# Performance work log

Measured on AMD Instinct MI355X. Metric: run time of the kernel, lower is better.

Reference implementation:

```python
import jax, jax.numpy as jnp
import numpy as np

KSIZE = 7
PAD = KSIZE // 2          # reflection pad radius
EPS_BN = 1e-5             # CONFIG.model.arch.batchnorm_eps
SCALE = 1.0               # self.scale
BN_W, BN_B = 0.1, 0.0     # BatchNorm init per module


def _l2n(x, eps=1e-12):
    return x / (jnp.linalg.norm(x) + eps)


def setup_inputs() -> dict:
    key = jax.random.key(0)
    ks = jax.random.split(key, 6)
    B, Cg, Co, H, W = 2, 128, 32, 512, 512
    f = jax.random.normal(ks[0], (B, Cg, H, W), jnp.float32)
    alpha = jax.random.normal(ks[1], (B, Co, H, W), jnp.float32)
    # guidance_conv: 1x1 conv Cg -> Cg//2 (xavier-ish init)
    wg = jax.random.normal(ks[2], (Cg // 2, Cg), jnp.float32) * (1.0 / np.sqrt(Cg))
    bg = jnp.zeros((Cg // 2,), jnp.float32)
    # spectral-norm 1x1 conv Co -> Co, no bias
    w_bar = jax.random.normal(ks[3], (Co, Co), jnp.float32) * (1.0 / np.sqrt(Co))
    u = _l2n(jax.random.normal(ks[4], (Co,), jnp.float32))
    v = _l2n(jax.random.normal(ks[5], (Co,), jnp.float32))
    return {"f": f, "alpha": alpha, "wg": wg, "bg": bg, "w_bar": w_bar, "u": u, "v": v}


def reference(f, alpha, wg, bg, w_bar, u, v):
    B, _, H, W = f.shape
    # 1x1 guidance conv
    g = jnp.einsum('oc,bchw->bohw', wg, f) + bg[None, :, None, None]
    # hop_normalize: channel-wise L2 normalize, clamped at 1e-4
    gn = g / jnp.maximum(jnp.linalg.norm(g, axis=1, keepdims=True), 1e-4)
    r = jnp.pad(gn, ((0, 0), (0, 0), (PAD, PAD), (PAD, PAD)), mode='reflect')
    # ksize^2 shifted-window correlation -> scores [K2, B, 1, H, W]
    scores = []
    for i in range(KSIZE):
        for j in range(KSIZE):
            if i == PAD and j == PAD:
                scores.append(jnp.full((B, 1, H, W), -10000.0, gn.dtype))
            else:
                scores.append((gn * r[:, :, i:i + H, j:j + W]).sum(axis=1, keepdims=True))
    s = jax.nn.softmax(jnp.stack(scores, axis=0) * SCALE, axis=0)
    # weighted neighborhood aggregation of alpha (skip center tap)
    alp = jnp.pad(alpha, ((0, 0), (0, 0), (PAD, PAD), (PAD, PAD)), mode='reflect')
    y = jnp.zeros_like(alpha)
    for i in range(KSIZE):
        for j in range(KSIZE):
            if i == PAD and j == PAD:
                continue
            y = y + alp[:, :, i:i + H, j:j + W] * s[i * KSIZE + j]
    # spectral-norm 1x1 conv (training: one detached power iteration)
    v1 = jax.lax.stop_gradient(_l2n(w_bar.T @ u))
    u1 = jax.lax.stop_gradient(_l2n(w_bar @ v1))
    sigma = u1 @ (w_bar @ v1)
    w_sn = w_bar / sigma
    y2 = jnp.einsum('oc,bchw->bohw', w_sn, y)
    # BatchNorm2d, training mode (batch stats), weight=0.1 bias=0
    mean = y2.mean(axis=(0, 2, 3), keepdims=True)
    var = y2.var(axis=(0, 2, 3), keepdims=True)
    y_bn = BN_W * (y2 - mean) / jnp.sqrt(var + EPS_BN) + BN_B
    return y_bn + alpha
```

## Files before the change

### kernel.cpp

```cpp
#include <hip/hip_runtime.h>

#define HWc   262144
#define CGc   128
#define CHc   64
#define COc   32
#define NPIXc 524288
#define TW 32
#define TH 8
#define HLW 38
#define HLH 14
#define HPX (HLW*HLH)

typedef _Float16 h2 __attribute__((ext_vector_type(2)));

__device__ __forceinline__ int refl(int p){
  if (p < 0) p = -p;
  else if (p >= 512) p = 1022 - p;
  return p;
}
__device__ __forceinline__ h2 as_h2(unsigned u){ union{unsigned u; h2 h;} x; x.u = u; return x.h; }
__device__ __forceinline__ unsigned as_u(h2 h){ union{unsigned u; h2 h;} x; x.h = h; return x.u; }
__device__ __forceinline__ unsigned pkh(float a, float b){
  h2 h; h.x = (_Float16)a; h.y = (_Float16)b; return as_u(h);
}
__device__ __forceinline__ float2 upk(unsigned u){
  h2 h = as_h2(u); return make_float2((float)h.x, (float)h.y);
}
__device__ __forceinline__ float dot2h(unsigned a, unsigned b, float c){
  return __builtin_amdgcn_fdot2(as_h2(a), as_h2(b), c, false);
}
__device__ __forceinline__ void mixlo(float& acc, unsigned ab, float e){
  asm("v_fma_mix_f32 %0, %1, %2, %0 op_sel:[0,0,0] op_sel_hi:[1,0,0]"
      : "+v"(acc) : "v"(ab), "v"(e));
}
__device__ __forceinline__ void mixhi(float& acc, unsigned ab, float e){
  asm("v_fma_mix_f32 %0, %1, %2, %0 op_sel:[1,0,0] op_sel_hi:[1,0,0]"
      : "+v"(acc) : "v"(ab), "v"(e));
}

__global__ void k0_prep(const float* __restrict__ wbar, const float* __restrict__ u,
                        const float* __restrict__ wg,
                        unsigned* __restrict__ wsnb, unsigned* __restrict__ wgb){
  const int t = threadIdx.x;
  __shared__ float sv1[32];
  float tv = 0.f;
  if (t < 32){
    #pragma unroll
    for (int o = 0; o < 32; o++) tv += wbar[o*32 + t] * u[o];
  }
  float sq = tv * tv;
  #pragma unroll
  for (int off = 32; off; off >>= 1) sq += __shfl_down(sq, off);
  const float n1 = sqrtf(__shfl(sq, 0)) + 1e-12f;
  if (t < 32) sv1[t] = tv / n1;
  __syncthreads();
  float tu = 0.f;
  if (t < 32){
    #pragma unroll
    for (int c = 0; c < 32; c++) tu += wbar[t*32 + c] * sv1[c];
  }
  float sq2 = tu * tu;
  #pragma unroll
  for (int off = 32; off; off >>= 1) sq2 += __shfl_down(sq2, off);
  const float S = __shfl(sq2, 0);
  const float inv = (sqrtf(S) + 1e-12f) / S;
  for (int k = t; k < 512; k += 64){
    const int o = k >> 4, p = k & 15;
    wsnb[k] = pkh(wbar[o*32 + 2*p] * inv, wbar[o*32 + 2*p + 1] * inv);
  }
  for (int k = t; k < 4096; k += 64){
    const int o = k >> 6, p = k & 63;
    wgb[k] = pkh(wg[o*128 + 2*p], wg[o*128 + 2*p + 1]);
  }
}

__global__ __launch_bounds__(256) void k1f(const float* __restrict__ f,
                                           const float* __restrict__ alpha,
                                           const unsigned* __restrict__ wgb,
                                           const unsigned* __restrict__ wsnb,
                                           const float* __restrict__ bg,
                                           unsigned* __restrict__ gn,
                                           unsigned* __restrict__ apm){
  const int p   = blockIdx.x * 256 + threadIdx.x;
  const int b   = p >> 18;
  const int pix = p & (HWc - 1);
  const float* fb = f + (size_t)b * CGc * HWc + pix;

  float acc[CHc];
  #pragma unroll
  for (int o = 0; o < CHc; o++) acc[o] = bg[o];

  #pragma unroll 1
  for (int pp = 0; pp < 64; pp += 4){
    unsigned fp[4];
    #pragma unroll
    for (int m = 0; m < 4; m++)
      fp[m] = pkh(fb[(size_t)(2*(pp+m)) * HWc], fb[(size_t)(2*(pp+m)+1) * HWc]);
    #pragma unroll
    for (int o = 0; o < CHc; o++){
      float a = acc[o];
      a = dot2h(fp[0], wgb[o*64 + pp + 0], a);
      a = dot2h(fp[1], wgb[o*64 + pp + 1], a);
      a = dot2h(fp[2], wgb[o*64 + pp + 2], a);
      a = dot2h(fp[3], wgb[o*64 + pp + 3], a);
      acc[o] = a;
    }
  }
  float nsq = 0.f;
  #pragma unroll
  for (int o = 0; o < CHc; o++) nsq = fmaf(acc[o], acc[o], nsq);
  const float inv = 1.f / fmaxf(sqrtf(nsq), 1e-4f);

  uint4* gp = (uint4*)(gn + (size_t)p * 32);
  #pragma unroll
  for (int k = 0; k < 8; k++){
    uint4 w;
    w.x = pkh(acc[8*k+0]*inv, acc[8*k+1]*inv);
    w.y = pkh(acc[8*k+2]*inv, acc[8*k+3]*inv);
    w.z = pkh(acc[8*k+4]*inv, acc[8*k+5]*inv);
    w.w = pkh(acc[8*k+6]*inv, acc[8*k+7]*inv);
    gp[k] = w;
  }

  const float* ab = alpha + (size_t)b * COc * HWc + pix;
  unsigned a16[16];
  #pragma unroll
  for (int k = 0; k < 16; k++)
    a16[k] = pkh(ab[(size_t)(2*k) * HWc], ab[(size_t)(2*k+1) * HWc]);
  unsigned ow[16];
  #pragma unroll
  for (int o = 0; o < COc; o += 2){
    float s0 = 0.f, s1 = 0.f;
    #pragma unroll
    for (int k = 0; k < 16; k++){
      s0 = dot2h(a16[k], wsnb[(o+0)*16 + k], s0);
      s1 = dot2h(a16[k], wsnb[(o+1)*16 + k], s1);
    }
    ow[o >> 1] = pkh(s0, s1);
  }
  uint4* op = (uint4*)(apm + (size_t)p * 16);
  #pragma unroll
  for (int k = 0; k < 4; k++)
    op[k] = make_uint4(ow[4*k], ow[4*k+1], ow[4*k+2], ow[4*k+3]);
}

__global__ __launch_bounds__(256) void k2_agg(const unsigned* __restrict__ gn,
                                              const unsigned* __restrict__ apm,
                                              unsigned* __restrict__ y2){
  __shared__ uint4 gs4[8][HPX];

  const int lb  = (blockIdx.x & 7) * 256 + (blockIdx.x >> 3);
  const int txx = lb & 15;
  const int tyy = (lb >> 4) & 63;
  const int bb  = lb >> 10;
  const int x0  = txx * TW, y0 = tyy * TH;
  const int tid = threadIdx.x;

  for (int t = tid; t < HPX; t += 256){
    const int hr = t / HLW;
    const int hc = t - hr * HLW;
    const int gy = refl(y0 + hr - 3);
    const int gx = refl(x0 + hc - 3);
    const uint4* src = (const uint4*)(gn + (size_t)((bb << 18) + (gy << 9) + gx) * 32);
    #pragma unroll
    for (int k = 0; k < 8; k++) gs4[k][t] = src[k];
  }
  __syncthreads();

  const int r  = tid >> 5, c = tid & 31;
  const int yy = y0 + r,  xx = x0 + c;
  const int self = (r + 3) * HLW + (c + 3);

  uint4 cv[8];
  #pragma unroll
  for (int k = 0; k < 8; k++) cv[k] = gs4[k][self];

  int ax[7];
  #pragma unroll
  for (int j = 0; j < 7; j++) ax[j] = refl(xx + j - 3);

  float yac[COc];
  #pragma unroll
  for (int k = 0; k < COc; k++) yac[k] = 0.f;
  float esum = 0.f;

  #pragma unroll 1
  for (int i = 0; i < 7; i++){
    const int ay = refl(yy + i - 3);
    const unsigned* aprow = apm + (size_t)((bb << 18) + (ay << 9)) * 16;
    const int rowbase = (r + i) * HLW + c;
    #pragma unroll
    for (int j = 0; j < 7; j++){
      if (i == 3 && j == 3) continue;
      const int hp = rowbase + j;
      float s0 = 0.f, s1 = 0.f, s2 = 0.f, s3 = 0.f;
      #pragma unroll
      for (int k = 0; k < 8; k++){
        const uint4 q = gs4[k][hp];
        s0 = dot2h(cv[k].x, q.x, s0);
        s1 = dot2h(cv[k].y, q.y, s1);
        s2 = dot2h(cv[k].z, q.z, s2);
        s3 = dot2h(cv[k].w, q.w, s3);
      }
      const float e = __expf((s0 + s1) + (s2 + s3));
      esum += e;
      const uint4* ap = (const uint4*)(aprow + (size_t)ax[j] * 16);
      #pragma unroll
      for (int kk = 0; kk < 4; kk++){
        const uint4 a = ap[kk];
        mixlo(yac[8*kk+0], a.x, e); mixhi(yac[8*kk+1], a.x, e);
        mixlo(yac[8*kk+2], a.y, e); mixhi(yac[8*kk+3], a.y, e);
        mixlo(yac[8*kk+4], a.z, e); mixhi(yac[8*kk+5], a.z, e);
        mixlo(yac[8*kk+6], a.w, e); mixhi(yac[8*kk+7], a.w, e);
      }
    }
  }

  const float inv = 1.f / esum;
  unsigned yw[16];
  #pragma unroll
  for (int k = 0; k < 16; k++) yw[k] = pkh(yac[2*k] * inv, yac[2*k+1] * inv);
  uint4* yp = (uint4*)(y2 + (size_t)((bb << 18) + (yy << 9) + xx) * 16);
  #pragma unroll
  for (int k = 0; k < 4; k++)
    yp[k] = make_uint4(yw[4*k], yw[4*k+1], yw[4*k+2], yw[4*k+3]);
}

__global__ __launch_bounds__(256) void k3_stats(const unsigned* __restrict__ y2,
                                                float* __restrict__ stats){
  float s[COc], q[COc];
  #pragma unroll
  for (int o = 0; o < COc; o++){ s[o] = 0.f; q[o] = 0.f; }
  const int stride = gridDim.x * 256;
  for (int p = blockIdx.x * 256 + threadIdx.x; p < NPIXc; p += stride){
    const uint4* yp = (const uint4*)(y2 + (size_t)p * 16);
    #pragma unroll
    for (int k = 0; k < 4; k++){
      const uint4 w = yp[k];
      const unsigned vv[4] = {w.x, w.y, w.z, w.w};
      #pragma unroll
      for (int m = 0; m < 4; m++){
        const float2 ab = upk(vv[m]);
        s[8*k+2*m]   += ab.x; q[8*k+2*m]   = fmaf(ab.x, ab.x, q[8*k+2*m]);
        s[8*k+2*m+1] += ab.y; q[8*k+2*m+1] = fmaf(ab.y, ab.y, q[8*k+2*m+1]);
      }
    }
  }
  #pragma unroll
  for (int o = 0; o < COc; o++){
    #pragma unroll
    for (int off = 32; off; off >>= 1){
      s[o] += __shfl_down(s[o], off);
      q[o] += __shfl_down(q[o], off);
    }
  }
  __shared__ float red[4][64];
  const int wv = threadIdx.x >> 6;
  if ((threadIdx.x & 63) == 0){
    #pragma unroll
    for (int o = 0; o < COc; o++){ red[wv][o] = s[o]; red[wv][32 + o] = q[o]; }
  }
  __syncthreads();
  if (threadIdx.x < 64){
    const float v = red[0][threadIdx.x] + red[1][threadIdx.x]
                  + red[2][threadIdx.x] + red[3][threadIdx.x];
    atomicAdd(&stats[threadIdx.x], v);
  }
}

__global__ void k3b_final(const float* __restrict__ stats, float* __restrict__ stats2){
  const int t = threadIdx.x;
  if (t < COc){
    const float invN = 1.f / (float)NPIXc;
    const float mean = stats[t] * invN;
    const float var  = fmaf(-mean, mean, stats[COc + t] * invN);
    stats2[t]       = mean;
    stats2[COc + t] = 0.1f * rsqrtf(var + 1e-5f);
  }
}

__global__ __launch_bounds__(256) void k4_out(const unsigned* __restrict__ y2,
                                              const float* __restrict__ alpha,
                                              const float* __restrict__ stats2,
                                              float* __restrict__ out){
  const int p   = blockIdx.x * 256 + threadIdx.x;
  const int b   = p >> 18;
  const int pix = p & (HWc - 1);
  const uint4* yp = (const uint4*)(y2 + (size_t)p * 16);
  const size_t boff = (size_t)b * COc * HWc + pix;
  #pragma unroll
  for (int k = 0; k < 4; k++){
    const uint4 w = yp[k];
    const unsigned vv[4] = {w.x, w.y, w.z, w.w};
    #pragma unroll
    for (int m = 0; m < 4; m++){
      const int o = 8*k + 2*m;
      const float2 ab = upk(vv[m]);
      out[boff + (size_t)o*HWc]     = fmaf(ab.x - stats2[o],   stats2[COc+o],
                                           alpha[boff + (size_t)o*HWc]);
      out[boff + (size_t)(o+1)*HWc] = fmaf(ab.y - stats2[o+1], stats2[COc+o+1],
                                           alpha[boff + (size_t)(o+1)*HWc]);
    }
  }
}

extern "C" void kernel_launch(void* const* d_in, const int* in_sizes, int n_in,
                              void* d_out, int out_size, void* d_ws, size_t ws_size,
                              hipStream_t stream){
  const float* f     = (const float*)d_in[0];
  const float* alpha = (const float*)d_in[1];
  const float* wg    = (const float*)d_in[2];
  const float* bg    = (const float*)d_in[3];
  const float* wbar  = (const float*)d_in[4];
  const float* u     = (const float*)d_in[5];
  (void)in_sizes; (void)n_in; (void)out_size; (void)ws_size;
  float* out = (float*)d_out;

  char* ws = (char*)d_ws;
  float*    stats  = (float*)ws;
  float*    stats2 = (float*)(ws + 4096);
  unsigned* wsnb   = (unsigned*)(ws + 8192);
  unsigned* wgb    = (unsigned*)(ws + 16384);
  unsigned* apm    = (unsigned*)(ws + 65536);
  unsigned* gn     = (unsigned*)(ws + 65536 + (size_t)NPIXc*64);
  unsigned* y2     = (unsigned*)(ws + 65536 + (size_t)NPIXc*64 + (size_t)NPIXc*128);

  hipMemsetAsync(stats, 0, 64 * sizeof(float), stream);
  k0_prep  <<<1, 64, 0, stream>>>(wbar, u, wg, wsnb, wgb);
  k1f      <<<NPIXc / 256, 256, 0, stream>>>(f, alpha, wgb, wsnb, bg, gn, apm);
  k2_agg   <<<2048, 256, 0, stream>>>(gn, apm, y2);
  k3_stats <<<256, 256, 0, stream>>>(y2, stats);
  k3b_final<<<1, 64, 0, stream>>>(stats, stats2);
  k4_out   <<<NPIXc / 256, 256, 0, stream>>>(y2, alpha, stats2, out);
}
```

Before: 328.3 us.

## Compute guidance and spectral-norm 1x1 convs with MFMA in k1

Replaces the per-thread fdot2 loops for the 128->64 guidance conv and the 32x32 spectral-norm conv with 16x16x32 f16 MFMA instructions. Weights are pre-swizzled into MFMA A-operand layout in k0_prep and held in registers, each wave processes 16-pixel tiles, and the channel L2 norm is reduced across lanes with shuffles. This removes the heavy VALU and scalar-weight-load cost of the per-pixel matvec, at the price of strided per-lane loads of f and alpha with only 16 contiguous pixels per row and narrower (uint2) output stores. It also switches the fp32-to-fp16 conversion of the inputs to round-toward-zero.

Measured after the change: 326.3 us. Within noise of the previous version (-0.6%).

```diff
diff --git a/kernel.cpp b/kernel.cpp
--- a/kernel.cpp
+++ b/kernel.cpp
@@ -11,7 +11,12 @@
 #define HLH 14
 #define HPX (HLW*HLH)
 
-typedef _Float16 h2 __attribute__((ext_vector_type(2)));
+typedef _Float16 h2    __attribute__((ext_vector_type(2)));
+typedef __fp16   fp2   __attribute__((ext_vector_type(2)));
+typedef _Float16 f16x8 __attribute__((ext_vector_type(8)));
+typedef float    f32x4 __attribute__((ext_vector_type(4)));
+
+union AB { uint4 q; f16x8 v; h2 p[4]; unsigned u[4]; };
 
 __device__ __forceinline__ int refl(int p){
   if (p < 0) p = -p;
@@ -23,6 +28,9 @@
 __device__ __forceinline__ unsigned pkh(float a, float b){
   h2 h; h.x = (_Float16)a; h.y = (_Float16)b; return as_u(h);
 }
+__device__ __forceinline__ h2 pkrtz(float a, float b){
+  union{ fp2 f; h2 h; } x; x.f = __builtin_amdgcn_cvt_pkrtz(a, b); return x.h;
+}
 __device__ __forceinline__ float2 upk(unsigned u){
   h2 h = as_h2(u); return make_float2((float)h.x, (float)h.y);
 }
@@ -40,7 +48,7 @@
 
 __global__ void k0_prep(const float* __restrict__ wbar, const float* __restrict__ u,
                         const float* __restrict__ wg,
-                        unsigned* __restrict__ wsnb, unsigned* __restrict__ wgb){
+                        unsigned* __restrict__ wgA, unsigned* __restrict__ wsnA){
   const int t = threadIdx.x;
   __shared__ float sv1[32];
   float tv = 0.f;
@@ -64,84 +72,107 @@
   for (int off = 32; off; off >>= 1) sq2 += __shfl_down(sq2, off);
   const float S = __shfl(sq2, 0);
   const float inv = (sqrtf(S) + 1e-12f) / S;
+
+  for (int k = t; k < 4096; k += 64){
+    const int mk = k >> 8, L = (k >> 2) & 63, j = k & 3;
+    const int m = mk >> 2, ks = mk & 3;
+    const int o = m*16 + (L & 15);
+    const int c = ks*32 + 8*(L >> 4) + 2*j;
+    wgA[k] = pkh(wg[o*128 + c], wg[o*128 + c + 1]);
+  }
   for (int k = t; k < 512; k += 64){
-    const int o = k >> 4, p = k & 15;
-    wsnb[k] = pkh(wbar[o*32 + 2*p] * inv, wbar[o*32 + 2*p + 1] * inv);
-  }
-  for (int k = t; k < 4096; k += 64){
-    const int o = k >> 6, p = k & 63;
-    wgb[k] = pkh(wg[o*128 + 2*p], wg[o*128 + 2*p + 1]);
-  }
-}
-
-__global__ __launch_bounds__(256) void k1f(const float* __restrict__ f,
+    const int m = k >> 8, L = (k >> 2) & 63, j = k & 3;
+    const int o = m*16 + (L & 15);
+    const int c = 8*(L >> 4) + 2*j;
+    wsnA[k] = pkh(wbar[o*32 + c] * inv, wbar[o*32 + c + 1] * inv);
+  }
+}
+
+__global__ __launch_bounds__(256) void k1m(const float* __restrict__ f,
                                            const float* __restrict__ alpha,
-                                           const unsigned* __restrict__ wgb,
-                                           const unsigned* __restrict__ wsnb,
+                                           const uint4* __restrict__ wgA,
+                                           const uint4* __restrict__ wsnA,
                                            const float* __restrict__ bg,
                                            unsigned* __restrict__ gn,
                                            unsigned* __restrict__ apm){
-  const int p   = blockIdx.x * 256 + threadIdx.x;
-  const int b   = p >> 18;
-  const int pix = p & (HWc - 1);
-  const float* fb = f + (size_t)b * CGc * HWc + pix;
-
-  float acc[CHc];
-  #pragma unroll
-  for (int o = 0; o < CHc; o++) acc[o] = bg[o];
+  const int tid  = threadIdx.x;
+  const int lane = tid & 63, w = tid >> 6;
+  const int lo   = lane & 15, hi = lane >> 4;
+
+  AB wga[4][4];
+  #pragma unroll
+  for (int m = 0; m < 4; m++)
+    #pragma unroll
+    for (int ks = 0; ks < 4; ks++)
+      wga[m][ks].q = wgA[(m*4 + ks)*64 + lane];
+  AB wsa[2];
+  #pragma unroll
+  for (int m = 0; m < 2; m++) wsa[m].q = wsnA[m*64 + lane];
+  float4 bgl[4];
+  #pragma unroll
+  for (int m = 0; m < 4; m++) bgl[m] = *(const float4*)(bg + m*16 + hi*4);
+
+  const int pxg = blockIdx.x * 256 + w * 64;
 
   #pragma unroll 1
-  for (int pp = 0; pp < 64; pp += 4){
-    unsigned fp[4];
-    #pragma unroll
-    for (int m = 0; m < 4; m++)
-      fp[m] = pkh(fb[(size_t)(2*(pp+m)) * HWc], fb[(size_t)(2*(pp+m)+1) * HWc]);
-    #pragma unroll
-    for (int o = 0; o < CHc; o++){
-      float a = acc[o];
-      a = dot2h(fp[0], wgb[o*64 + pp + 0], a);
-      a = dot2h(fp[1], wgb[o*64 + pp + 1], a);
-      a = dot2h(fp[2], wgb[o*64 + pp + 2], a);
-      a = dot2h(fp[3], wgb[o*64 + pp + 3], a);
-      acc[o] = a;
-    }
-  }
-  float nsq = 0.f;
-  #pragma unroll
-  for (int o = 0; o < CHc; o++) nsq = fmaf(acc[o], acc[o], nsq);
-  const float inv = 1.f / fmaxf(sqrtf(nsq), 1e-4f);
-
-  uint4* gp = (uint4*)(gn + (size_t)p * 32);
-  #pragma unroll
-  for (int k = 0; k < 8; k++){
-    uint4 w;
-    w.x = pkh(acc[8*k+0]*inv, acc[8*k+1]*inv);
-    w.y = pkh(acc[8*k+2]*inv, acc[8*k+3]*inv);
-    w.z = pkh(acc[8*k+4]*inv, acc[8*k+5]*inv);
-    w.w = pkh(acc[8*k+6]*inv, acc[8*k+7]*inv);
-    gp[k] = w;
-  }
-
-  const float* ab = alpha + (size_t)b * COc * HWc + pix;
-  unsigned a16[16];
-  #pragma unroll
-  for (int k = 0; k < 16; k++)
-    a16[k] = pkh(ab[(size_t)(2*k) * HWc], ab[(size_t)(2*k+1) * HWc]);
-  unsigned ow[16];
-  #pragma unroll
-  for (int o = 0; o < COc; o += 2){
-    float s0 = 0.f, s1 = 0.f;
-    #pragma unroll
-    for (int k = 0; k < 16; k++){
-      s0 = dot2h(a16[k], wsnb[(o+0)*16 + k], s0);
-      s1 = dot2h(a16[k], wsnb[(o+1)*16 + k], s1);
-    }
-    ow[o >> 1] = pkh(s0, s1);
-  }
-  uint4* op = (uint4*)(apm + (size_t)p * 16);
-  #pragma unroll
-  for (int k = 0; k < 4; k++)
-    op[k] = make_uint4(ow[4*k], ow[4*k+1], ow[4*k+2], ow[4*k+3]);
+  for (int nt = 0; nt < 4; nt++){
+    const int px0  = pxg + nt*16;
+    const int b    = px0 >> 18;
+    const int pix0 = px0 & (HWc - 1);
+    const float* fb = f + (size_t)b * CGc * HWc + pix0 + lo;
+
+    f32x4 acc[4];
+    #pragma unroll
+    for (int m = 0; m < 4; m++) acc[m] = (f32x4){0.f, 0.f, 0.f, 0.f};
+
+    #pragma unroll
+    for (int ks = 0; ks < 4; ks++){
+      const float* fc = fb + (size_t)(ks*32 + hi*8) * HWc;
+      AB bf;
+      #pragma unroll
+      for (int j = 0; j < 4; j++)
+        bf.p[j] = pkrtz(fc[(size_t)(2*j) * HWc], fc[(size_t)(2*j + 1) * HWc]);
+      #pragma unroll
+      for (int m = 0; m < 4; m++)
+        acc[m] = __builtin_amdgcn_mfma_f32_16x16x32_f16(wga[m][ks].v, bf.v, acc[m], 0, 0, 0);
+    }
+
+    float v[16]; float nsq = 0.f;
+    #pragma unroll
+    for (int m = 0; m < 4; m++){
+      v[4*m+0] = acc[m][0] + bgl[m].x;
+      v[4*m+1] = acc[m][1] + bgl[m].y;
+      v[4*m+2] = acc[m][2] + bgl[m].z;
+      v[4*m+3] = acc[m][3] + bgl[m].w;
+      nsq = fmaf(v[4*m+0], v[4*m+0], nsq); nsq = fmaf(v[4*m+1], v[4*m+1], nsq);
+      nsq = fmaf(v[4*m+2], v[4*m+2], nsq); nsq = fmaf(v[4*m+3], v[4*m+3], nsq);
+    }
+    nsq += __shfl_xor(nsq, 16);
+    nsq += __shfl_xor(nsq, 32);
+    const float inv = 1.f / fmaxf(sqrtf(nsq), 1e-4f);
+
+    unsigned* gp = gn + (size_t)(px0 + lo) * 32 + hi*2;
+    #pragma unroll
+    for (int m = 0; m < 4; m++){
+      uint2 st = make_uint2(pkh(v[4*m+0]*inv, v[4*m+1]*inv),
+                            pkh(v[4*m+2]*inv, v[4*m+3]*inv));
+      *(uint2*)(gp + m*8) = st;
+    }
+
+    const float* ac = alpha + (size_t)b * COc * HWc + pix0 + lo + (size_t)(hi*8) * HWc;
+    AB af;
+    #pragma unroll
+    for (int j = 0; j < 4; j++)
+      af.p[j] = pkrtz(ac[(size_t)(2*j) * HWc], ac[(size_t)(2*j + 1) * HWc]);
+    unsigned* op = apm + (size_t)(px0 + lo) * 16 + hi*2;
+    #pragma unroll
+    for (int m = 0; m < 2; m++){
+      f32x4 aa = (f32x4){0.f, 0.f, 0.f, 0.f};
+      aa = __builtin_amdgcn_mfma_f32_16x16x32_f16(wsa[m].v, af.v, aa, 0, 0, 0);
+      uint2 st = make_uint2(pkh(aa[0], aa[1]), pkh(aa[2], aa[3]));
+      *(uint2*)(op + m*8) = st;
+    }
+  }
 }
 
 __global__ __launch_bounds__(256) void k2_agg(const unsigned* __restrict__ gn,
@@ -319,15 +350,16 @@
   char* ws = (char*)d_ws;
   float*    stats  = (float*)ws;
   float*    stats2 = (float*)(ws + 4096);
-  unsigned* wsnb   = (unsigned*)(ws + 8192);
-  unsigned* wgb    = (unsigned*)(ws + 16384);
+  unsigned* wgA    = (unsigned*)(ws + 8192);
+  unsigned* wsnA   = (unsigned*)(ws + 32768);
   unsigned* apm    = (unsigned*)(ws + 65536);
   unsigned* gn     = (unsigned*)(ws + 65536 + (size_t)NPIXc*64);
   unsigned* y2     = (unsigned*)(ws + 65536 + (size_t)NPIXc*64 + (size_t)NPIXc*128);
 
-  hipMemsetAsync(stats, 0, 64 * sizeof(float), stream);
-  k0_prep  <<<1, 64, 0, stream>>>(wbar, u, wg, wsnb, wgb);
-  k1f      <<<NPIXc / 256, 256, 0, stream>>>(f, alpha, wgb, wsnb, bg, gn, apm);
+  (void)hipMemsetAsync(stats, 0, 64 * sizeof(float), stream);
+  k0_prep  <<<1, 64, 0, stream>>>(wbar, u, wg, wgA, wsnA);
+  k1m      <<<NPIXc / 256, 256, 0, stream>>>(f, alpha, (const uint4*)wgA,
+                                             (const uint4*)wsnA, bg, gn, apm);
   k2_agg   <<<2048, 256, 0, stream>>>(gn, apm, y2);
   k3_stats <<<256, 256, 0, stream>>>(y2, stats);
   k3b_final<<<1, 64, 0, stream>>>(stats, stats2);
```
